# Performance work log

Measured on AMD Instinct MI355X. Metric: run time of the kernel, lower is better.

Reference implementation:

```python
import jax, jax.numpy as jnp
import numpy as np

B, C, H, W = 4, 256, 64, 64


def setup_inputs() -> dict:
    key = jax.random.key(0)
    k1, k2, k3, k4 = jax.random.split(key, 4)
    inp = jax.random.normal(k1, (B, C, H, W), dtype=jnp.float32)
    inter_mask = jnp.ones((B, 1, H, W), dtype=jnp.float32)
    flow_init = jax.random.normal(k2, (B, 2, H, W), dtype=jnp.float32)
    # nn.Linear(C, C): weight [out,in], bias [out]
    lim = 1.0 / np.sqrt(C)
    W_lin = jax.random.uniform(k3, (C, C), dtype=jnp.float32, minval=-lim, maxval=lim)
    b_lin = jax.random.uniform(k4, (C,), dtype=jnp.float32, minval=-lim, maxval=lim)
    return {"inp": inp, "inter_mask": inter_mask, "flow_init": flow_init,
            "W_lin": W_lin, "b_lin": b_lin}


def reference(inp, inter_mask, flow_init, W_lin, b_lin):
    batch, ch, ht, wd = inp.shape
    n = ht * wd
    # [B, N, C]
    x = inp.reshape(batch, ch, n).transpose(0, 2, 1)
    x = x @ W_lin.T + b_lin
    scale = ch ** (-0.5)
    # [B, N, N] full self-correlation
    scores = jnp.einsum('bnc,bmc->bnm', x * scale, x)
    attn = jax.nn.softmax(scores, axis=-1)
    # [B, N, 2]
    flow = flow_init.reshape(batch, 2, n).transpose(0, 2, 1)
    flow_add = attn @ flow
    # [B, 2, H, W]
    return flow_add.reshape(batch, ht, wd, 2).transpose(0, 3, 1, 2)
```

## Files before the change

kernel.cpp:

```cpp
#include <hip/hip_runtime.h>
#include <hip/hip_bf16.h>

#define NB 4
#define CCH 256
#define NN 4096
#define QT 128
#define KSPLIT 4
#define MRANGE (NN / KSPLIT)
#define MTILE 64
#define NTILES (MRANGE / MTILE)
#define VPAD 8

#define SQRTK 0.30028060f

typedef __attribute__((ext_vector_type(8))) short short8;
typedef __attribute__((ext_vector_type(16))) float f32x16;
typedef __attribute__((ext_vector_type(4))) int i32x4;

__device__ inline ushort f2bf(float f) {
    uint u = __float_as_uint(f);
    uint r = (u + 0x7fffu + ((u >> 16) & 1u)) >> 16;
    return (ushort)r;
}

__device__ inline float dev_exp2(float x) {
#if __has_builtin(__builtin_amdgcn_exp2f)
    return __builtin_amdgcn_exp2f(x);
#else
    return exp2f(x);
#endif
}

__device__ inline void gl_lds16(const void* g, void* l) {
    __builtin_amdgcn_global_load_lds(
        (const __attribute__((address_space(1))) unsigned int*)g,
        (__attribute__((address_space(3))) unsigned int*)l, 16, 0, 0);
}

__global__ __launch_bounds__(256) void transp_k(const float* __restrict__ inp,
                                                ushort* __restrict__ inpT,
                                                const float* __restrict__ W,
                                                ushort* __restrict__ Wb) {
    if (blockIdx.x >= 1024) {
        int i = (blockIdx.x - 1024) * 256 + threadIdx.x;
        float4 v = reinterpret_cast<const float4*>(W)[i];
        ushort4 r;
        r.x = f2bf(v.x); r.y = f2bf(v.y); r.z = f2bf(v.z); r.w = f2bf(v.w);
        reinterpret_cast<ushort4*>(Wb)[i] = r;
        return;
    }
    int wg = blockIdx.x;
    int nblk = wg & 63, cblk = (wg >> 6) & 3, b = wg >> 8;
    __shared__ float tile[64 * 67];
    int t = threadIdx.x;
    const float* src = inp + ((size_t)(b * CCH + cblk * 64)) * NN + nblk * 64;
#pragma unroll
    for (int p = 0; p < 4; p++) {
        int ci = p * 256 + t;
        int c = ci >> 4, n4 = ci & 15;
        float4 v = *reinterpret_cast<const float4*>(src + (size_t)c * NN + n4 * 4);
        float* d = &tile[c * 67 + n4 * 4];
        d[0] = v.x; d[1] = v.y; d[2] = v.z; d[3] = v.w;
    }
    __syncthreads();
    ushort* dst = inpT + ((size_t)(b * NN + nblk * 64)) * CCH + cblk * 64;
#pragma unroll
    for (int p = 0; p < 2; p++) {
        int u = p * 256 + t;
        int n = u >> 3, cc = u & 7;
        ushort tmp[8];
#pragma unroll
        for (int j = 0; j < 8; j++) tmp[j] = f2bf(tile[(cc * 8 + j) * 67 + n]);
        uint4 o;
        o.x = (uint)tmp[0] | ((uint)tmp[1] << 16);
        o.y = (uint)tmp[2] | ((uint)tmp[3] << 16);
        o.z = (uint)tmp[4] | ((uint)tmp[5] << 16);
        o.w = (uint)tmp[6] | ((uint)tmp[7] << 16);
        *reinterpret_cast<uint4*>(dst + (size_t)n * CCH + cc * 8) = o;
    }
}

__global__ __launch_bounds__(256) void linear_k(const ushort* __restrict__ inpT,
                                                const ushort* __restrict__ Wb,
                                                const float* __restrict__ bias,
                                                ushort* __restrict__ xs) {
    int wg = blockIdx.x;
    int b = wg >> 6, nt = wg & 63;
    int t = threadIdx.x, l = t & 63, w = t >> 6;
    int nbase = nt * 64 + (w & 1) * 32;
    int obase = (w >> 1) * 128;
    const ushort* arow = inpT + ((size_t)(b * NN + nbase + (l & 31))) * CCH + ((l >> 5) * 8);
    const ushort* wrow = Wb + ((size_t)(obase + (l & 31))) * CCH + ((l >> 5) * 8);
    f32x16 acc[4];
#pragma unroll
    for (int os = 0; os < 4; os++)
#pragma unroll
        for (int r = 0; r < 16; r++) acc[os][r] = 0.f;

#pragma unroll
    for (int ch = 0; ch < 16; ch++) {
        short8 a = *reinterpret_cast<const short8*>(arow + ch * 16);
#pragma unroll
        for (int os = 0; os < 4; os++) {
            short8 bb = *reinterpret_cast<const short8*>(wrow + (size_t)os * 32 * CCH + ch * 16);
            acc[os] = __builtin_amdgcn_mfma_f32_32x32x16_bf16(a, bb, acc[os], 0, 0, 0);
        }
    }
#pragma unroll
    for (int os = 0; os < 4; os++) {
        int oc = obase + os * 32 + (l & 31);
        float bv = bias[oc];
#pragma unroll
        for (int r = 0; r < 16; r++) {
            int row = (r & 3) + 8 * (r >> 2) + 4 * (l >> 5);
            float v = (acc[os][r] + bv) * SQRTK;
            xs[((size_t)(b * NN + nt * 64 + (w & 1) * 32 + row)) * CCH + oc] = f2bf(v);
        }
    }
}

__global__ __launch_bounds__(256) void attn_k(const ushort* __restrict__ xs,
                                              const float* __restrict__ flow,
                                              float* __restrict__ part) {
    int wg = blockIdx.x;
    int b = wg >> 7;
    int qt = (wg >> 2) & 31;
    int ks = wg & 3;
    int t = threadIdx.x, l = t & 63, w = t >> 6;
    const ushort* xb = xs + (size_t)b * NN * CCH;
    int qbase = qt * QT + w * 32;
    int mstart = ks * MRANGE;

    __shared__ ushort kt[2][MTILE * 256];
    __shared__ ushort vlds[4][MRANGE + VPAD];

    {
        int m0 = t * 4;
        float4 fx4 = *reinterpret_cast<const float4*>(flow + (size_t)b * 2 * NN + mstart + m0);
        float4 fy4 = *reinterpret_cast<const float4*>(flow + (size_t)b * 2 * NN + NN + mstart + m0);
        float fxv[4] = {fx4.x, fx4.y, fx4.z, fx4.w};
        float fyv[4] = {fy4.x, fy4.y, fy4.z, fy4.w};
#pragma unroll
        for (int i = 0; i < 4; i++) {
            int m = m0 + i, ml = m & 15;
            int pos = (m & ~15) | (ml & 3) | ((ml & 4) << 1) | ((ml & 8) >> 1);
            vlds[0][pos] = f2bf(fxv[i]);
            vlds[1][pos] = f2bf(fyv[i]);
            vlds[2][pos] = 0x3F80;
            vlds[3][pos] = 0;
        }
    }

    short8 qf[16];
    const ushort* qrow = xb + ((size_t)(qbase + (l & 31))) * CCH + (l >> 5) * 8;
#pragma unroll
    for (int ch = 0; ch < 16; ch++)
        qf[ch] = *reinterpret_cast<const short8*>(qrow + ch * 16);

    f32x16 pv;
#pragma unroll
    for (int r = 0; r < 16; r++) pv[r] = 0.f;

    auto stage = [&](int buf, int tile) {
        int mb = mstart + tile * MTILE;
        const char* src = (const char*)(xb + (size_t)mb * CCH);
#pragma unroll
        for (int p = 0; p < 8; p++) {
            int chunk = w * 8 + p;
            int lin = chunk * 1024 + l * 16;
            int row = lin >> 9;
            int cb = lin & 511;
            int gsw = cb ^ ((row & 15) << 4);
            gl_lds16(src + (size_t)row * 512 + gsw, &kt[buf][chunk * 512]);
        }
    };

    int c_sel = (l & 31) < 3 ? (l & 31) : 3;
    stage(0, 0);
    __syncthreads();
    int cur = 0;
    for (int tile = 0; tile < NTILES; tile++) {
        if (tile + 1 < NTILES) stage(cur ^ 1, tile + 1);
#pragma unroll
        for (int ms = 0; ms < 2; ms++) {
            f32x16 S;
#pragma unroll
            for (int r = 0; r < 16; r++) S[r] = 0.f;
            const char* base = (const char*)&kt[cur][(ms * 32 + (l & 31)) * 256];
            int swz = (l & 15) << 4;
#pragma unroll
            for (int ch = 0; ch < 16; ch++) {
                int cbyte = (ch * 32 + ((l >> 5) * 16)) ^ swz;
                short8 kf = *reinterpret_cast<const short8*>(base + cbyte);
                S = __builtin_amdgcn_mfma_f32_32x32x16_bf16(kf, qf[ch], S, 0, 0, 0);
            }
#pragma unroll
            for (int r = 0; r < 16; r++) S[r] = dev_exp2(S[r]);
            uint wd[8];
#pragma unroll
            for (int p = 0; p < 8; p++) {
                float lo = S[2 * p], hi = S[2 * p + 1];
                asm("v_cvt_pk_bf16_f32 %0, %1, %2" : "=v"(wd[p]) : "v"(lo), "v"(hi));
            }
            i32x4 lo4 = {(int)wd[0], (int)wd[1], (int)wd[2], (int)wd[3]};
            i32x4 hi4 = {(int)wd[4], (int)wd[5], (int)wd[6], (int)wd[7]};
            short8 pa0 = __builtin_bit_cast(short8, lo4);
            short8 pa1 = __builtin_bit_cast(short8, hi4);
            int mloc = tile * MTILE + ms * 32;
            const ushort* vb = &vlds[c_sel][mloc + (l >> 5) * 8];
            short8 v0 = *reinterpret_cast<const short8*>(vb);
            short8 v1 = *reinterpret_cast<const short8*>(vb + 16);
            pv = __builtin_amdgcn_mfma_f32_32x32x16_bf16(pa0, v0, pv, 0, 0, 0);
            pv = __builtin_amdgcn_mfma_f32_32x32x16_bf16(pa1, v1, pv, 0, 0, 0);
        }
        __syncthreads();
        cur ^= 1;
    }

    int c = l & 31;
    if (c < 3) {
        float* pb = part + ((size_t)(b * KSPLIT + ks)) * 3 * NN;
        int off = ((c + 1) % 3) * NN;
#pragma unroll
        for (int r = 0; r < 16; r++) {
            int row = (r & 3) + 8 * (r >> 2) + 4 * (l >> 5);
            pb[off + qbase + row] = pv[r];
        }
    }
}

__global__ void finalize_k(const float* __restrict__ part, float* __restrict__ out) {
    int i = blockIdx.x * 256 + threadIdx.x;
    int b = i >> 12, n = i & 4095;
    float s = 0.f, x = 0.f, y = 0.f;
#pragma unroll
    for (int ks = 0; ks < KSPLIT; ks++) {
        const float* p = part + ((size_t)(b * KSPLIT + ks)) * 3 * NN;
        s += p[n];
        x += p[NN + n];
        y += p[2 * NN + n];
    }
    out[(size_t)b * 2 * NN + n] = x / s;
    out[(size_t)b * 2 * NN + NN + n] = y / s;
}

extern "C" void kernel_launch(void* const* d_in, const int* in_sizes, int n_in,
                              void* d_out, int out_size, void* d_ws, size_t ws_size,
                              hipStream_t stream) {
    const float* inp  = (const float*)d_in[0];
    const float* flow = (const float*)d_in[2];
    const float* W    = (const float*)d_in[3];
    const float* bias = (const float*)d_in[4];
    float* out = (float*)d_out;

    char* ws = (char*)d_ws;
    ushort* xs   = (ushort*)(ws);
    ushort* inpT = (ushort*)(ws + 8388608);
    ushort* Wb   = (ushort*)(ws + 16777216);
    float*  part = (float*)(ws + 8388608);

    transp_k<<<1088, 256, 0, stream>>>(inp, inpT, W, Wb);
    linear_k<<<256, 256, 0, stream>>>(inpT, Wb, bias, xs);
    attn_k<<<512, 256, 0, stream>>>(xs, flow, part);
    finalize_k<<<64, 256, 0, stream>>>(part, out);
}
```

Before: 65.79 us.

## Software-pipeline QK and exp/PV across tiles, double key split

The attention kernel now computes the next tile's QK^T scores while it exponentiates and accumulates the current tile, using a prefetch two tiles ahead and two independent PV accumulators. The key range is split 8 ways instead of 4 with 32-row tiles, which doubles the grid and halves LDS per block, and launch bounds request two blocks per CU. The aim is to hide exp and MFMA dependency latency and raise occupancy. In exchange, finalize does more partial-sum traffic and register pressure rises from the extra accumulator and the in-flight score tile.

```diff
diff --git a/kernel.cpp b/kernel.cpp
--- a/kernel.cpp
+++ b/kernel.cpp
@@ -5,9 +5,9 @@
 #define CCH 256
 #define NN 4096
 #define QT 128
-#define KSPLIT 4
+#define KSPLIT 8
 #define MRANGE (NN / KSPLIT)
-#define MTILE 64
+#define MTILE 32
 #define NTILES (MRANGE / MTILE)
 #define VPAD 8
 
@@ -119,13 +119,13 @@
     }
 }
 
-__global__ __launch_bounds__(256) void attn_k(const ushort* __restrict__ xs,
-                                              const float* __restrict__ flow,
-                                              float* __restrict__ part) {
+__global__ __launch_bounds__(256, 2) void attn_k(const ushort* __restrict__ xs,
+                                                 const float* __restrict__ flow,
+                                                 float* __restrict__ part) {
     int wg = blockIdx.x;
-    int b = wg >> 7;
-    int qt = (wg >> 2) & 31;
-    int ks = wg & 3;
+    int b = wg >> 8;
+    int qt = (wg >> 3) & 31;
+    int ks = wg & 7;
     int t = threadIdx.x, l = t & 63, w = t >> 6;
     const ushort* xb = xs + (size_t)b * NN * CCH;
     int qbase = qt * QT + w * 32;
@@ -135,13 +135,13 @@
     __shared__ ushort vlds[4][MRANGE + VPAD];
 
     {
-        int m0 = t * 4;
-        float4 fx4 = *reinterpret_cast<const float4*>(flow + (size_t)b * 2 * NN + mstart + m0);
-        float4 fy4 = *reinterpret_cast<const float4*>(flow + (size_t)b * 2 * NN + NN + mstart + m0);
-        float fxv[4] = {fx4.x, fx4.y, fx4.z, fx4.w};
-        float fyv[4] = {fy4.x, fy4.y, fy4.z, fy4.w};
-#pragma unroll
-        for (int i = 0; i < 4; i++) {
+        int m0 = t * 2;
+        float2 fx2 = *reinterpret_cast<const float2*>(flow + (size_t)b * 2 * NN + mstart + m0);
+        float2 fy2 = *reinterpret_cast<const float2*>(flow + (size_t)b * 2 * NN + NN + mstart + m0);
+        float fxv[2] = {fx2.x, fx2.y};
+        float fyv[2] = {fy2.x, fy2.y};
+#pragma unroll
+        for (int i = 0; i < 2; i++) {
             int m = m0 + i, ml = m & 15;
             int pos = (m & ~15) | (ml & 3) | ((ml & 4) << 1) | ((ml & 8) >> 1);
             vlds[0][pos] = f2bf(fxv[i]);
@@ -157,16 +157,16 @@
     for (int ch = 0; ch < 16; ch++)
         qf[ch] = *reinterpret_cast<const short8*>(qrow + ch * 16);
 
-    f32x16 pv;
-#pragma unroll
-    for (int r = 0; r < 16; r++) pv[r] = 0.f;
+    f32x16 pvA, pvB;
+#pragma unroll
+    for (int r = 0; r < 16; r++) { pvA[r] = 0.f; pvB[r] = 0.f; }
 
     auto stage = [&](int buf, int tile) {
         int mb = mstart + tile * MTILE;
         const char* src = (const char*)(xb + (size_t)mb * CCH);
 #pragma unroll
-        for (int p = 0; p < 8; p++) {
-            int chunk = w * 8 + p;
+        for (int p = 0; p < 4; p++) {
+            int chunk = w * 4 + p;
             int lin = chunk * 1024 + l * 16;
             int row = lin >> 9;
             int cb = lin & 511;
@@ -175,46 +175,52 @@
         }
     };
 
+    auto qk = [&](int buf, f32x16& S) {
+#pragma unroll
+        for (int r = 0; r < 16; r++) S[r] = 0.f;
+        const char* base = (const char*)&kt[buf][(l & 31) * 256];
+        int swz = (l & 15) << 4;
+#pragma unroll
+        for (int ch = 0; ch < 16; ch++) {
+            int cbyte = (ch * 32 + ((l >> 5) * 16)) ^ swz;
+            short8 kf = *reinterpret_cast<const short8*>(base + cbyte);
+            S = __builtin_amdgcn_mfma_f32_32x32x16_bf16(kf, qf[ch], S, 0, 0, 0);
+        }
+    };
+
     int c_sel = (l & 31) < 3 ? (l & 31) : 3;
+
     stage(0, 0);
     __syncthreads();
-    int cur = 0;
+    f32x16 Sp;
+    qk(0, Sp);
+    stage(1, 1);
+
+#pragma unroll 2
     for (int tile = 0; tile < NTILES; tile++) {
-        if (tile + 1 < NTILES) stage(cur ^ 1, tile + 1);
-#pragma unroll
-        for (int ms = 0; ms < 2; ms++) {
-            f32x16 S;
-#pragma unroll
-            for (int r = 0; r < 16; r++) S[r] = 0.f;
-            const char* base = (const char*)&kt[cur][(ms * 32 + (l & 31)) * 256];
-            int swz = (l & 15) << 4;
-#pragma unroll
-            for (int ch = 0; ch < 16; ch++) {
-                int cbyte = (ch * 32 + ((l >> 5) * 16)) ^ swz;
-                short8 kf = *reinterpret_cast<const short8*>(base + cbyte);
-                S = __builtin_amdgcn_mfma_f32_32x32x16_bf16(kf, qf[ch], S, 0, 0, 0);
-            }
-#pragma unroll
-            for (int r = 0; r < 16; r++) S[r] = dev_exp2(S[r]);
-            uint wd[8];
-#pragma unroll
-            for (int p = 0; p < 8; p++) {
-                float lo = S[2 * p], hi = S[2 * p + 1];
-                asm("v_cvt_pk_bf16_f32 %0, %1, %2" : "=v"(wd[p]) : "v"(lo), "v"(hi));
-            }
-            i32x4 lo4 = {(int)wd[0], (int)wd[1], (int)wd[2], (int)wd[3]};
-            i32x4 hi4 = {(int)wd[4], (int)wd[5], (int)wd[6], (int)wd[7]};
-            short8 pa0 = __builtin_bit_cast(short8, lo4);
-            short8 pa1 = __builtin_bit_cast(short8, hi4);
-            int mloc = tile * MTILE + ms * 32;
-            const ushort* vb = &vlds[c_sel][mloc + (l >> 5) * 8];
-            short8 v0 = *reinterpret_cast<const short8*>(vb);
-            short8 v1 = *reinterpret_cast<const short8*>(vb + 16);
-            pv = __builtin_amdgcn_mfma_f32_32x32x16_bf16(pa0, v0, pv, 0, 0, 0);
-            pv = __builtin_amdgcn_mfma_f32_32x32x16_bf16(pa1, v1, pv, 0, 0, 0);
-        }
         __syncthreads();
-        cur ^= 1;
+        f32x16 Sn;
+        if (tile + 1 < NTILES) qk((tile + 1) & 1, Sn);
+        if (tile + 2 < NTILES) stage(tile & 1, tile + 2);
+
+#pragma unroll
+        for (int r = 0; r < 16; r++) Sp[r] = dev_exp2(Sp[r]);
+        uint wd[8];
+#pragma unroll
+        for (int p = 0; p < 8; p++) {
+            asm("v_cvt_pk_bf16_f32 %0, %1, %2" : "=v"(wd[p]) : "v"(Sp[2 * p]), "v"(Sp[2 * p + 1]));
+        }
+        i32x4 lo4 = {(int)wd[0], (int)wd[1], (int)wd[2], (int)wd[3]};
+        i32x4 hi4 = {(int)wd[4], (int)wd[5], (int)wd[6], (int)wd[7]};
+        short8 pa0 = __builtin_bit_cast(short8, lo4);
+        short8 pa1 = __builtin_bit_cast(short8, hi4);
+        const ushort* vb = &vlds[c_sel][tile * MTILE + (l >> 5) * 8];
+        short8 v0 = *reinterpret_cast<const short8*>(vb);
+        short8 v1 = *reinterpret_cast<const short8*>(vb + 16);
+        pvA = __builtin_amdgcn_mfma_f32_32x32x16_bf16(pa0, v0, pvA, 0, 0, 0);
+        pvB = __builtin_amdgcn_mfma_f32_32x32x16_bf16(pa1, v1, pvB, 0, 0, 0);
+
+        Sp = Sn;
     }
 
     int c = l & 31;
@@ -224,7 +230,7 @@
 #pragma unroll
         for (int r = 0; r < 16; r++) {
             int row = (r & 3) + 8 * (r >> 2) + 4 * (l >> 5);
-            pb[off + qbase + row] = pv[r];
+            pb[off + qbase + row] = pvA[r] + pvB[r];
         }
     }
 }
@@ -261,6 +267,6 @@
 
     transp_k<<<1088, 256, 0, stream>>>(inp, inpT, W, Wb);
     linear_k<<<256, 256, 0, stream>>>(inpT, Wb, bias, xs);
-    attn_k<<<512, 256, 0, stream>>>(xs, flow, part);
+    attn_k<<<1024, 256, 0, stream>>>(xs, flow, part);
     finalize_k<<<64, 256, 0, stream>>>(part, out);
 }
```

Result: no change. 65.88 us (+0.1%).
